# Optimization experiments

Measured on AMD Instinct MI355X. Metric: run time of the kernel, lower is better.

The kernel has to match this reference:

```python
import jax, jax.numpy as jnp
import numpy as np

N_NODES = 100000
FEAT_DIM = 256
MAX_DEG = 128
BATCH = 512          # per side (batch1, batch2)
S1 = 10              # layer-2 fanout (1-hop samples)
S2 = 25              # layer-1 fanout (2-hop samples)
HID = 256            # per-branch output dim; concat -> 512


def setup_inputs() -> dict:
    key = jax.random.key(0)
    ks = jax.random.split(key, 10)
    return {
        "features": jax.random.normal(ks[0], (N_NODES, FEAT_DIM), jnp.float32),
        "Ws1": jax.random.normal(ks[1], (FEAT_DIM, HID), jnp.float32) * 0.05,
        "Wn1": jax.random.normal(ks[2], (FEAT_DIM, HID), jnp.float32) * 0.05,
        "Ws2": jax.random.normal(ks[3], (2 * HID, HID), jnp.float32) * 0.05,
        "Wn2": jax.random.normal(ks[4], (2 * HID, HID), jnp.float32) * 0.05,
        "adj": jax.random.randint(ks[5], (N_NODES, MAX_DEG), 0, N_NODES, jnp.int32),
        "batch1": jax.random.randint(ks[6], (BATCH,), 0, N_NODES, jnp.int32),
        "batch2": jax.random.randint(ks[7], (BATCH,), 0, N_NODES, jnp.int32),
        "col1": jax.random.randint(ks[8], (2 * BATCH, S1), 0, MAX_DEG, jnp.int32),
        "col2": jax.random.randint(ks[9], (2 * BATCH * S1, S2), 0, MAX_DEG, jnp.int32),
    }


def _l2_normalize(x, eps=1e-12):
    return x * jax.lax.rsqrt(jnp.maximum(jnp.sum(x * x, axis=1, keepdims=True), eps))


def _mean_agg(h_self, h_neigh, fanout, Ws, Wn, act):
    # h_self: [M, d_in]; h_neigh: [M*fanout, d_in]
    neigh_mean = h_neigh.reshape(h_self.shape[0], fanout, -1).mean(axis=1)
    return act(jnp.concatenate([h_self @ Ws, neigh_mean @ Wn], axis=1))


def reference(features, Ws1, Wn1, Ws2, Wn2, adj, batch1, batch2, col1, col2):
    nodes = jnp.concatenate([batch1, batch2])                  # [2B]
    # uniform neighbor sampling via gather into preprocessed adjacency table
    s1 = jnp.take_along_axis(adj[nodes], col1, axis=1).reshape(-1)   # [2B*S1]
    s2 = jnp.take_along_axis(adj[s1], col2, axis=1).reshape(-1)      # [2B*S1*S2]
    h0 = features[nodes]      # [2B, D]
    h1 = features[s1]         # [2B*S1, D]
    h2 = features[s2]         # [2B*S1*S2, D]
    # GraphSAGE layer 1 (relu, concat)
    h0_new = _mean_agg(h0, h1, S1, Ws1, Wn1, jax.nn.relu)      # [2B, 2H]
    h1_new = _mean_agg(h1, h2, S2, Ws1, Wn1, jax.nn.relu)      # [2B*S1, 2H]
    # GraphSAGE layer 2 (identity act, concat)
    out = _mean_agg(h0_new, h1_new, S1, Ws2, Wn2, lambda x: x)  # [2B, 2H]
    out = _l2_normalize(out)
    return out  # rows [:BATCH] = outputs1, rows [BATCH:] = outputs2
```

## Files before the change

kernel.cpp:

```cpp
#include <hip/hip_runtime.h>
#include <hip/hip_bf16.h>

#define NB2    1024
#define FS1    10
#define FS2    25
#define FD     256
#define FH     256
#define MAXDEG 128

typedef __attribute__((ext_vector_type(8))) short bf16x8;
typedef __attribute__((ext_vector_type(4))) float f32x4;

__device__ inline ushort f2bf(float f) {
    union { float f; unsigned u; } v; v.f = f;
    unsigned u = v.u;
    unsigned r = (u + 0x7FFFu + ((u >> 16) & 1u)) >> 16;
    return (ushort)r;
}
__device__ inline float bf2f(ushort h) {
    union { unsigned u; float f; } v; v.u = ((unsigned)h) << 16;
    return v.f;
}

__global__ void prep_kernel(const float* __restrict__ Ws1, const float* __restrict__ Wn1,
                            const float* __restrict__ Ws2, const float* __restrict__ Wn2,
                            ushort* __restrict__ Wt_s1, ushort* __restrict__ Wt_n1,
                            ushort* __restrict__ Wt_s2, ushort* __restrict__ Wt_n2,
                            const int* __restrict__ batch1, const int* __restrict__ batch2,
                            const int* __restrict__ adj,
                            const int* __restrict__ col1, const int* __restrict__ col2,
                            int* __restrict__ nodes, int* __restrict__ s1,
                            int* __restrict__ s2)
{
    int b = blockIdx.x;
    if (b < 1536) {
        int t = b * 256 + threadIdx.x;
        const float* W; ushort* Wt; int K; int base;
        if (t < 131072) {
            K = 256;
            if (t < 65536) { W = Ws1; Wt = Wt_s1; base = 0; }
            else           { W = Wn1; Wt = Wt_n1; base = 65536; }
        } else {
            K = 512;
            if (t < 262144) { W = Ws2; Wt = Wt_s2; base = 131072; }
            else            { W = Wn2; Wt = Wt_n2; base = 262144; }
        }
        int tt = t - base;
        int k = tt >> 8;
        int n = tt & 255;
        Wt[(long)n * K + k] = f2bf(W[tt]);
    } else {
        int t2 = (b - 1536) * 256 + threadIdx.x;
        int i  = t2 / FS2;
        int ns = i / FS1;
        int node = (ns < 512) ? batch1[ns] : batch2[ns - 512];
        int s1v = adj[(long)node * MAXDEG + col1[i]];
        s2[t2] = adj[(long)s1v * MAXDEG + col2[t2]];
        if (t2 - i * FS2 == 0) {
            s1[i] = s1v;
            if (i - ns * FS1 == 0) nodes[ns] = node;
        }
    }
}

template<int F>
__device__ __forceinline__ void mean_body(const float* __restrict__ src,
                                          const int* __restrict__ idx,
                                          ushort* __restrict__ dst,
                                          int g, int l)
{
    const int* ip = idx + (long)g * F;
    int r[F];
    #pragma unroll
    for (int j = 0; j < F; ++j) r[j] = ip[j];

    float4 acc[4];
    #pragma unroll
    for (int q = 0; q < 4; ++q) acc[q] = make_float4(0.f, 0.f, 0.f, 0.f);

    #pragma unroll
    for (int j0 = 0; j0 < F; j0 += 8) {
        float4 v[8];
        #pragma unroll
        for (int u = 0; u < 8; ++u)
            if (j0 + u < F)
                v[u] = *((const float4*)(src + (long)r[j0 + u] * FD) + l);
        #pragma unroll
        for (int u = 0; u < 8; ++u)
            if (j0 + u < F) {
                int q = u & 3;
                acc[q].x += v[u].x; acc[q].y += v[u].y;
                acc[q].z += v[u].z; acc[q].w += v[u].w;
            }
    }
    float s = 1.0f / F;
    float sx = (acc[0].x + acc[1].x + acc[2].x + acc[3].x) * s;
    float sy = (acc[0].y + acc[1].y + acc[2].y + acc[3].y) * s;
    float sz = (acc[0].z + acc[1].z + acc[2].z + acc[3].z) * s;
    float sw = (acc[0].w + acc[1].w + acc[2].w + acc[3].w) * s;
    uint2 o;
    o.x = (unsigned)f2bf(sx) | ((unsigned)f2bf(sy) << 16);
    o.y = (unsigned)f2bf(sz) | ((unsigned)f2bf(sw) << 16);
    *((uint2*)(dst + (long)g * FD) + l) = o;
}

__device__ __forceinline__ void l1gemm_self_wave(const float* __restrict__ features,
                                                 const int* __restrict__ idx,
                                                 const ushort* __restrict__ Bt,
                                                 ushort* __restrict__ C,
                                                 int r0, int cs, int coff,
                                                 int m16, int g)
{
    const int row = r0 + m16;
    const long arow = (long)idx[row];

    f32x4 acc[4];
    #pragma unroll
    for (int j = 0; j < 4; ++j) acc[j] = (f32x4){0.f, 0.f, 0.f, 0.f};

    #pragma unroll
    for (int k0 = 0; k0 < 256; k0 += 32) {
        const float* p = features + arow * FD + k0 + g * 8;
        float4 v0 = *(const float4*)p;
        float4 v1 = *(const float4*)(p + 4);
        bf16x8 a;
        a[0] = (short)f2bf(v0.x); a[1] = (short)f2bf(v0.y);
        a[2] = (short)f2bf(v0.z); a[3] = (short)f2bf(v0.w);
        a[4] = (short)f2bf(v1.x); a[5] = (short)f2bf(v1.y);
        a[6] = (short)f2bf(v1.z); a[7] = (short)f2bf(v1.w);
        #pragma unroll
        for (int j = 0; j < 4; ++j) {
            bf16x8 bf = *(const bf16x8*)(Bt + (long)(cs * 64 + j * 16 + m16) * 256 + k0 + g * 8);
            acc[j] = __builtin_amdgcn_mfma_f32_16x16x32_bf16(a, bf, acc[j], 0, 0, 0);
        }
    }
    #pragma unroll
    for (int j = 0; j < 4; ++j)
        #pragma unroll
        for (int r = 0; r < 4; ++r)
            C[(long)(r0 + g * 4 + r) * 512 + coff + cs * 64 + j * 16 + m16] =
                f2bf(fmaxf(acc[j][r], 0.f));
}

__device__ __forceinline__ void l1gemm_neigh_wave(const ushort* __restrict__ An,
                                                  const ushort* __restrict__ Bt,
                                                  ushort* __restrict__ C,
                                                  int r0, int cs, int coff,
                                                  int m16, int g)
{
    const int row = r0 + m16;
    f32x4 acc[4];
    #pragma unroll
    for (int j = 0; j < 4; ++j) acc[j] = (f32x4){0.f, 0.f, 0.f, 0.f};

    #pragma unroll
    for (int k0 = 0; k0 < 256; k0 += 32) {
        bf16x8 a = *(const bf16x8*)(An + (long)row * FD + k0 + g * 8);
        #pragma unroll
        for (int j = 0; j < 4; ++j) {
            bf16x8 bf = *(const bf16x8*)(Bt + (long)(cs * 64 + j * 16 + m16) * 256 + k0 + g * 8);
            acc[j] = __builtin_amdgcn_mfma_f32_16x16x32_bf16(a, bf, acc[j], 0, 0, 0);
        }
    }
    #pragma unroll
    for (int j = 0; j < 4; ++j)
        #pragma unroll
        for (int r = 0; r < 4; ++r)
            C[(long)(r0 + g * 4 + r) * 512 + coff + cs * 64 + j * 16 + m16] =
                f2bf(fmaxf(acc[j][r], 0.f));
}

__device__ __forceinline__ void l2gemm_wave(const ushort* __restrict__ A,
                                            const ushort* __restrict__ Bt,
                                            float* __restrict__ op,
                                            int r0, int cs, int kh, int coff,
                                            int m16, int g)
{
    const int row = r0 + m16;
    const int kb  = kh * 128;
    f32x4 acc[4];
    #pragma unroll
    for (int j = 0; j < 4; ++j) acc[j] = (f32x4){0.f, 0.f, 0.f, 0.f};

    #pragma unroll
    for (int ks = 0; ks < 128; ks += 32) {
        int k = kb + ks;
        bf16x8 a = *(const bf16x8*)(A + (long)row * 512 + k + g * 8);
        #pragma unroll
        for (int j = 0; j < 4; ++j) {
            bf16x8 bf = *(const bf16x8*)(Bt + (long)(cs * 64 + j * 16 + m16) * 512 + k + g * 8);
            acc[j] = __builtin_amdgcn_mfma_f32_16x16x32_bf16(a, bf, acc[j], 0, 0, 0);
        }
    }
    #pragma unroll
    for (int j = 0; j < 4; ++j)
        #pragma unroll
        for (int r = 0; r < 4; ++r)
            op[(long)(r0 + g * 4 + r) * 512 + coff + cs * 64 + j * 16 + m16] = acc[j][r];
}

__global__ void k2_means_l1self(const float* __restrict__ features,
                                const int* __restrict__ s2, const int* __restrict__ s1,
                                const int* __restrict__ nodes,
                                ushort* __restrict__ nm2, ushort* __restrict__ nm1,
                                const ushort* __restrict__ Wt_s1,
                                ushort* __restrict__ h1n, ushort* __restrict__ h0n)
{
    int b = blockIdx.x;
    int wave = threadIdx.x >> 6;
    int l = threadIdx.x & 63;
    if (b < 2560) { mean_body<FS2>(features, s2, nm2, b * 4 + wave, l); return; }
    if (b < 2816) { mean_body<FS1>(features, s1, nm1, (b - 2816 + 256) * 4 + wave, l); return; }
    int u = (b - 2816) * 4 + wave;
    int cs = u & 3;
    int t = u >> 2;
    int m16 = l & 15, g = l >> 4;
    if (t < 640) l1gemm_self_wave(features, s1,    Wt_s1, h1n, t * 16,        cs, 0, m16, g);
    else         l1gemm_self_wave(features, nodes, Wt_s1, h0n, (t - 640) * 16, cs, 0, m16, g);
}

__global__ void k3_l1neigh(const ushort* __restrict__ nm2, const ushort* __restrict__ nm1,
                           const ushort* __restrict__ Wt_n1,
                           ushort* __restrict__ h1n, ushort* __restrict__ h0n)
{
    int u = blockIdx.x * 4 + (threadIdx.x >> 6);
    int l = threadIdx.x & 63;
    int cs = u & 3;
    int t = u >> 2;
    int m16 = l & 15, g = l >> 4;
    if (t < 640) l1gemm_neigh_wave(nm2, Wt_n1, h1n, t * 16,        cs, 256, m16, g);
    else         l1gemm_neigh_wave(nm1, Wt_n1, h0n, (t - 640) * 16, cs, 256, m16, g);
}

__global__ void k4_ml2_l2self(const ushort* __restrict__ h1n, ushort* __restrict__ ml2,
                              const ushort* __restrict__ h0n,
                              const ushort* __restrict__ Wt_s2,
                              float* __restrict__ opre)
{
    int b = blockIdx.x;
    int wave = threadIdx.x >> 6;
    int l = threadIdx.x & 63;
    if (b < 256) {
        int gp = b * 4 + wave;
        float acc[8] = {};
        for (int j = 0; j < FS1; ++j) {
            uint4 v = *((const uint4*)(h1n + ((long)gp * FS1 + j) * 512) + l);
            unsigned wd[4] = { v.x, v.y, v.z, v.w };
            #pragma unroll
            for (int q = 0; q < 4; ++q) {
                acc[2 * q]     += bf2f((ushort)(wd[q] & 0xFFFF));
                acc[2 * q + 1] += bf2f((ushort)(wd[q] >> 16));
            }
        }
        float s = 1.0f / FS1;
        uint4 o;
        unsigned* ow = (unsigned*)&o;
        #pragma unroll
        for (int q = 0; q < 4; ++q)
            ow[q] = (unsigned)f2bf(acc[2 * q] * s) | ((unsigned)f2bf(acc[2 * q + 1] * s) << 16);
        *((uint4*)(ml2 + (long)gp * 512) + l) = o;
        return;
    }
    int u = (b - 256) * 4 + wave;
    int kh = u & 3, cs = (u >> 2) & 3, rt = u >> 4;
    int m16 = l & 15, g = l >> 4;
    l2gemm_wave(h0n, Wt_s2, opre + (long)kh * NB2 * 512, rt * 16, cs, kh, 0, m16, g);
}

__global__ void k5_l2neigh(const ushort* __restrict__ ml2,
                           const ushort* __restrict__ Wt_n2,
                           float* __restrict__ opre)
{
    int u = blockIdx.x * 4 + (threadIdx.x >> 6);
    int l = threadIdx.x & 63;
    int kh = u & 3, cs = (u >> 2) & 3, rt = u >> 4;
    int m16 = l & 15, g = l >> 4;
    l2gemm_wave(ml2, Wt_n2, opre + (long)kh * NB2 * 512, rt * 16, cs, kh, 256, m16, g);
}

__global__ void l2norm_kernel(const float* __restrict__ in, float* __restrict__ out)
{
    int r = blockIdx.x;
    int t = threadIdx.x;
    long i0 = (long)r * 512 + t;
    const long P = (long)NB2 * 512;
    float v0 = in[i0]       + in[i0 + P]       + in[i0 + 2*P]       + in[i0 + 3*P];
    float v1 = in[i0 + 256] + in[i0 + P + 256] + in[i0 + 2*P + 256] + in[i0 + 3*P + 256];
    float s = v0 * v0 + v1 * v1;
    #pragma unroll
    for (int o = 32; o > 0; o >>= 1) s += __shfl_down(s, o, 64);
    __shared__ float wsum[4];
    if ((t & 63) == 0) wsum[t >> 6] = s;
    __syncthreads();
    float tot = wsum[0] + wsum[1] + wsum[2] + wsum[3];
    float inv = rsqrtf(fmaxf(tot, 1e-12f));
    out[r * 512 + t] = v0 * inv;
    out[r * 512 + 256 + t] = v1 * inv;
}

extern "C" void kernel_launch(void* const* d_in, const int* in_sizes, int n_in,
                              void* d_out, int out_size, void* d_ws, size_t ws_size,
                              hipStream_t stream)
{
    const float* features = (const float*)d_in[0];
    const float* Ws1      = (const float*)d_in[1];
    const float* Wn1      = (const float*)d_in[2];
    const float* Ws2      = (const float*)d_in[3];
    const float* Wn2      = (const float*)d_in[4];
    const int*   adj      = (const int*)d_in[5];
    const int*   batch1   = (const int*)d_in[6];
    const int*   batch2   = (const int*)d_in[7];
    const int*   col1     = (const int*)d_in[8];
    const int*   col2     = (const int*)d_in[9];
    float* out = (float*)d_out;

    char* w = (char*)d_ws;
    auto alloc = [&](size_t bytes) {
        char* p = w;
        w += (bytes + 255) & ~(size_t)255;
        return p;
    };
    int*    nodes = (int*)alloc((size_t)NB2 * 4);
    int*    s1    = (int*)alloc((size_t)NB2 * FS1 * 4);
    int*    s2    = (int*)alloc((size_t)NB2 * FS1 * FS2 * 4);
    ushort* nm1   = (ushort*)alloc((size_t)NB2 * FD * 2);
    ushort* nm2   = (ushort*)alloc((size_t)NB2 * FS1 * FD * 2);
    ushort* h0n   = (ushort*)alloc((size_t)NB2 * 512 * 2);
    ushort* h1n   = (ushort*)alloc((size_t)NB2 * FS1 * 512 * 2);
    ushort* ml2   = (ushort*)alloc((size_t)NB2 * 512 * 2);
    float*  opre  = (float*)alloc((size_t)4 * NB2 * 512 * 4);
    ushort* Wt_s1 = (ushort*)alloc((size_t)FD * FH * 2);
    ushort* Wt_n1 = (ushort*)alloc((size_t)FD * FH * 2);
    ushort* Wt_s2 = (ushort*)alloc((size_t)512 * FH * 2);
    ushort* Wt_n2 = (ushort*)alloc((size_t)512 * FH * 2);

    prep_kernel<<<2536, 256, 0, stream>>>(Ws1, Wn1, Ws2, Wn2,
                                          Wt_s1, Wt_n1, Wt_s2, Wt_n2,
                                          batch1, batch2, adj, col1, col2,
                                          nodes, s1, s2);

    k2_means_l1self<<<3520, 256, 0, stream>>>(features, s2, s1, nodes,
                                              nm2, nm1, Wt_s1, h1n, h0n);

    k3_l1neigh<<<704, 256, 0, stream>>>(nm2, nm1, Wt_n1, h1n, h0n);

    k4_ml2_l2self<<<512, 256, 0, stream>>>(h1n, ml2, h0n, Wt_s2, opre);

    k5_l2neigh<<<256, 256, 0, stream>>>(ml2, Wt_n2, opre);

    l2norm_kernel<<<NB2, 256, 0, stream>>>(opre, out);
}
```

Baseline: 98.68 us.

## Pre-convert feature table to bf16 and fuse layer-2 neighbor mean into GEMM

The prep kernel now converts the whole 100000x256 fp32 feature table to bf16 on every call. The mean and self-GEMM gathers then read half as many bytes and skip the per-element conversion. Separately, the layer-2 neighbor mean is computed inside the neighbor GEMM, with both layer-2 GEMMs in one kernel, which removes the ml2 buffer and one launch. The trade-off is a full-table read and write in the prep kernel, which is far more traffic than the gathers it saves. Neighbor means are also now summed from bf16-rounded inputs rather than fp32.

```diff
diff --git a/kernel.cpp b/kernel.cpp
--- a/kernel.cpp
+++ b/kernel.cpp
@@ -22,7 +22,8 @@
     return v.f;
 }
 
-__global__ void prep_kernel(const float* __restrict__ Ws1, const float* __restrict__ Wn1,
+__global__ void prep_kernel(const float* __restrict__ features, ushort* __restrict__ fbf,
+                            const float* __restrict__ Ws1, const float* __restrict__ Wn1,
                             const float* __restrict__ Ws2, const float* __restrict__ Wn2,
                             ushort* __restrict__ Wt_s1, ushort* __restrict__ Wt_n1,
                             ushort* __restrict__ Wt_s2, ushort* __restrict__ Wt_n2,
@@ -33,8 +34,15 @@
                             int* __restrict__ s2)
 {
     int b = blockIdx.x;
-    if (b < 1536) {
-        int t = b * 256 + threadIdx.x;
+    if (b < 25000) {
+        long t = (long)b * 256 + threadIdx.x;
+        float4 v = ((const float4*)features)[t];
+        uint2 o;
+        o.x = (unsigned)f2bf(v.x) | ((unsigned)f2bf(v.y) << 16);
+        o.y = (unsigned)f2bf(v.z) | ((unsigned)f2bf(v.w) << 16);
+        ((uint2*)fbf)[t] = o;
+    } else if (b < 26536) {
+        int t = (b - 25000) * 256 + threadIdx.x;
         const float* W; ushort* Wt; int K; int base;
         if (t < 131072) {
             K = 256;
@@ -50,7 +58,7 @@
         int n = tt & 255;
         Wt[(long)n * K + k] = f2bf(W[tt]);
     } else {
-        int t2 = (b - 1536) * 256 + threadIdx.x;
+        int t2 = (b - 26536) * 256 + threadIdx.x;
         int i  = t2 / FS2;
         int ns = i / FS1;
         int node = (ns < 512) ? batch1[ns] : batch2[ns - 512];
@@ -64,7 +72,7 @@
 }
 
 template<int F>
-__device__ __forceinline__ void mean_body(const float* __restrict__ src,
+__device__ __forceinline__ void mean_body(const ushort* __restrict__ src,
                                           const int* __restrict__ idx,
                                           ushort* __restrict__ dst,
                                           int g, int l)
@@ -74,37 +82,32 @@
     #pragma unroll
     for (int j = 0; j < F; ++j) r[j] = ip[j];
 
-    float4 acc[4];
-    #pragma unroll
-    for (int q = 0; q < 4; ++q) acc[q] = make_float4(0.f, 0.f, 0.f, 0.f);
+    float acc[4] = {0.f, 0.f, 0.f, 0.f};
 
     #pragma unroll
     for (int j0 = 0; j0 < F; j0 += 8) {
-        float4 v[8];
+        uint2 v[8];
         #pragma unroll
         for (int u = 0; u < 8; ++u)
             if (j0 + u < F)
-                v[u] = *((const float4*)(src + (long)r[j0 + u] * FD) + l);
+                v[u] = *((const uint2*)(src + (long)r[j0 + u] * FD) + l);
         #pragma unroll
         for (int u = 0; u < 8; ++u)
             if (j0 + u < F) {
-                int q = u & 3;
-                acc[q].x += v[u].x; acc[q].y += v[u].y;
-                acc[q].z += v[u].z; acc[q].w += v[u].w;
+                acc[0] += bf2f((ushort)(v[u].x & 0xFFFF));
+                acc[1] += bf2f((ushort)(v[u].x >> 16));
+                acc[2] += bf2f((ushort)(v[u].y & 0xFFFF));
+                acc[3] += bf2f((ushort)(v[u].y >> 16));
             }
     }
     float s = 1.0f / F;
-    float sx = (acc[0].x + acc[1].x + acc[2].x + acc[3].x) * s;
-    float sy = (acc[0].y + acc[1].y + acc[2].y + acc[3].y) * s;
-    float sz = (acc[0].z + acc[1].z + acc[2].z + acc[3].z) * s;
-    float sw = (acc[0].w + acc[1].w + acc[2].w + acc[3].w) * s;
     uint2 o;
-    o.x = (unsigned)f2bf(sx) | ((unsigned)f2bf(sy) << 16);
-    o.y = (unsigned)f2bf(sz) | ((unsigned)f2bf(sw) << 16);
+    o.x = (unsigned)f2bf(acc[0] * s) | ((unsigned)f2bf(acc[1] * s) << 16);
+    o.y = (unsigned)f2bf(acc[2] * s) | ((unsigned)f2bf(acc[3] * s) << 16);
     *((uint2*)(dst + (long)g * FD) + l) = o;
 }
 
-__device__ __forceinline__ void l1gemm_self_wave(const float* __restrict__ features,
+__device__ __forceinline__ void l1gemm_self_wave(const ushort* __restrict__ fbf,
                                                  const int* __restrict__ idx,
                                                  const ushort* __restrict__ Bt,
                                                  ushort* __restrict__ C,
@@ -120,14 +123,7 @@
 
     #pragma unroll
     for (int k0 = 0; k0 < 256; k0 += 32) {
-        const float* p = features + arow * FD + k0 + g * 8;
-        float4 v0 = *(const float4*)p;
-        float4 v1 = *(const float4*)(p + 4);
-        bf16x8 a;
-        a[0] = (short)f2bf(v0.x); a[1] = (short)f2bf(v0.y);
-        a[2] = (short)f2bf(v0.z); a[3] = (short)f2bf(v0.w);
-        a[4] = (short)f2bf(v1.x); a[5] = (short)f2bf(v1.y);
-        a[6] = (short)f2bf(v1.z); a[7] = (short)f2bf(v1.w);
+        bf16x8 a = *(const bf16x8*)(fbf + arow * FD + k0 + g * 8);
         #pragma unroll
         for (int j = 0; j < 4; ++j) {
             bf16x8 bf = *(const bf16x8*)(Bt + (long)(cs * 64 + j * 16 + m16) * 256 + k0 + g * 8);
@@ -199,7 +195,7 @@
             op[(long)(r0 + g * 4 + r) * 512 + coff + cs * 64 + j * 16 + m16] = acc[j][r];
 }
 
-__global__ void k2_means_l1self(const float* __restrict__ features,
+__global__ void k2_means_l1self(const ushort* __restrict__ fbf,
                                 const int* __restrict__ s2, const int* __restrict__ s1,
                                 const int* __restrict__ nodes,
                                 ushort* __restrict__ nm2, ushort* __restrict__ nm1,
@@ -209,14 +205,14 @@
     int b = blockIdx.x;
     int wave = threadIdx.x >> 6;
     int l = threadIdx.x & 63;
-    if (b < 2560) { mean_body<FS2>(features, s2, nm2, b * 4 + wave, l); return; }
-    if (b < 2816) { mean_body<FS1>(features, s1, nm1, (b - 2816 + 256) * 4 + wave, l); return; }
+    if (b < 2560) { mean_body<FS2>(fbf, s2, nm2, b * 4 + wave, l); return; }
+    if (b < 2816) { mean_body<FS1>(fbf, s1, nm1, (b - 2560) * 4 + wave, l); return; }
     int u = (b - 2816) * 4 + wave;
     int cs = u & 3;
     int t = u >> 2;
     int m16 = l & 15, g = l >> 4;
-    if (t < 640) l1gemm_self_wave(features, s1,    Wt_s1, h1n, t * 16,        cs, 0, m16, g);
-    else         l1gemm_self_wave(features, nodes, Wt_s1, h0n, (t - 640) * 16, cs, 0, m16, g);
+    if (t < 640) l1gemm_self_wave(fbf, s1,    Wt_s1, h1n, t * 16,         cs, 0, m16, g);
+    else         l1gemm_self_wave(fbf, nodes, Wt_s1, h0n, (t - 640) * 16, cs, 0, m16, g);
 }
 
 __global__ void k3_l1neigh(const ushort* __restrict__ nm2, const ushort* __restrict__ nm1,
@@ -228,54 +224,63 @@
     int cs = u & 3;
     int t = u >> 2;
     int m16 = l & 15, g = l >> 4;
-    if (t < 640) l1gemm_neigh_wave(nm2, Wt_n1, h1n, t * 16,        cs, 256, m16, g);
+    if (t < 640) l1gemm_neigh_wave(nm2, Wt_n1, h1n, t * 16,         cs, 256, m16, g);
     else         l1gemm_neigh_wave(nm1, Wt_n1, h0n, (t - 640) * 16, cs, 256, m16, g);
 }
 
-__global__ void k4_ml2_l2self(const ushort* __restrict__ h1n, ushort* __restrict__ ml2,
-                              const ushort* __restrict__ h0n,
-                              const ushort* __restrict__ Wt_s2,
-                              float* __restrict__ opre)
+__global__ void k4_l2both(const ushort* __restrict__ h1n, const ushort* __restrict__ h0n,
+                          const ushort* __restrict__ Wt_s2, const ushort* __restrict__ Wt_n2,
+                          float* __restrict__ opre)
 {
     int b = blockIdx.x;
     int wave = threadIdx.x >> 6;
     int l = threadIdx.x & 63;
+    int m16 = l & 15, g = l >> 4;
     if (b < 256) {
-        int gp = b * 4 + wave;
-        float acc[8] = {};
+        int u = b * 4 + wave;
+        int kh = u & 3, cs = (u >> 2) & 3, rt = u >> 4;
+        l2gemm_wave(h0n, Wt_s2, opre + (long)kh * NB2 * 512, rt * 16, cs, kh, 0, m16, g);
+        return;
+    }
+    int u = (b - 256) * 4 + wave;
+    int kh = u & 3, cs = (u >> 2) & 3, rt = u >> 4;
+    const int r0  = rt * 16;
+    const int row = r0 + m16;
+    const int kb  = kh * 128;
+
+    f32x4 acc[4];
+    #pragma unroll
+    for (int j = 0; j < 4; ++j) acc[j] = (f32x4){0.f, 0.f, 0.f, 0.f};
+
+    #pragma unroll
+    for (int ks = 0; ks < 128; ks += 32) {
+        int k = kb + ks;
+        float a8[8] = {};
+        #pragma unroll
         for (int j = 0; j < FS1; ++j) {
-            uint4 v = *((const uint4*)(h1n + ((long)gp * FS1 + j) * 512) + l);
+            uint4 v = *(const uint4*)(h1n + ((long)row * FS1 + j) * 512 + k + g * 8);
             unsigned wd[4] = { v.x, v.y, v.z, v.w };
             #pragma unroll
             for (int q = 0; q < 4; ++q) {
-                acc[2 * q]     += bf2f((ushort)(wd[q] & 0xFFFF));
-                acc[2 * q + 1] += bf2f((ushort)(wd[q] >> 16));
+                a8[2 * q]     += bf2f((ushort)(wd[q] & 0xFFFF));
+                a8[2 * q + 1] += bf2f((ushort)(wd[q] >> 16));
             }
         }
-        float s = 1.0f / FS1;
-        uint4 o;
-        unsigned* ow = (unsigned*)&o;
-        #pragma unroll
-        for (int q = 0; q < 4; ++q)
-            ow[q] = (unsigned)f2bf(acc[2 * q] * s) | ((unsigned)f2bf(acc[2 * q + 1] * s) << 16);
-        *((uint4*)(ml2 + (long)gp * 512) + l) = o;
-        return;
-    }
-    int u = (b - 256) * 4 + wave;
-    int kh = u & 3, cs = (u >> 2) & 3, rt = u >> 4;
-    int m16 = l & 15, g = l >> 4;
-    l2gemm_wave(h0n, Wt_s2, opre + (long)kh * NB2 * 512, rt * 16, cs, kh, 0, m16, g);
-}
-
-__global__ void k5_l2neigh(const ushort* __restrict__ ml2,
-                           const ushort* __restrict__ Wt_n2,
-                           float* __restrict__ opre)
-{
-    int u = blockIdx.x * 4 + (threadIdx.x >> 6);
-    int l = threadIdx.x & 63;
-    int kh = u & 3, cs = (u >> 2) & 3, rt = u >> 4;
-    int m16 = l & 15, g = l >> 4;
-    l2gemm_wave(ml2, Wt_n2, opre + (long)kh * NB2 * 512, rt * 16, cs, kh, 256, m16, g);
+        bf16x8 a;
+        #pragma unroll
+        for (int q = 0; q < 8; ++q) a[q] = (short)f2bf(a8[q] * (1.0f / FS1));
+        #pragma unroll
+        for (int j = 0; j < 4; ++j) {
+            bf16x8 bf = *(const bf16x8*)(Wt_n2 + (long)(cs * 64 + j * 16 + m16) * 512 + k + g * 8);
+            acc[j] = __builtin_amdgcn_mfma_f32_16x16x32_bf16(a, bf, acc[j], 0, 0, 0);
+        }
+    }
+    float* op = opre + (long)kh * NB2 * 512;
+    #pragma unroll
+    for (int j = 0; j < 4; ++j)
+        #pragma unroll
+        for (int r = 0; r < 4; ++r)
+            op[(long)(r0 + g * 4 + r) * 512 + 256 + cs * 64 + j * 16 + m16] = acc[j][r];
 }
 
 __global__ void l2norm_kernel(const float* __restrict__ in, float* __restrict__ out)
@@ -320,6 +325,7 @@
         w += (bytes + 255) & ~(size_t)255;
         return p;
     };
+    ushort* fbf   = (ushort*)alloc((size_t)100000 * FD * 2);
     int*    nodes = (int*)alloc((size_t)NB2 * 4);
     int*    s1    = (int*)alloc((size_t)NB2 * FS1 * 4);
     int*    s2    = (int*)alloc((size_t)NB2 * FS1 * FS2 * 4);
@@ -327,26 +333,23 @@
     ushort* nm2   = (ushort*)alloc((size_t)NB2 * FS1 * FD * 2);
     ushort* h0n   = (ushort*)alloc((size_t)NB2 * 512 * 2);
     ushort* h1n   = (ushort*)alloc((size_t)NB2 * FS1 * 512 * 2);
-    ushort* ml2   = (ushort*)alloc((size_t)NB2 * 512 * 2);
     float*  opre  = (float*)alloc((size_t)4 * NB2 * 512 * 4);
     ushort* Wt_s1 = (ushort*)alloc((size_t)FD * FH * 2);
     ushort* Wt_n1 = (ushort*)alloc((size_t)FD * FH * 2);
     ushort* Wt_s2 = (ushort*)alloc((size_t)512 * FH * 2);
     ushort* Wt_n2 = (ushort*)alloc((size_t)512 * FH * 2);
 
-    prep_kernel<<<2536, 256, 0, stream>>>(Ws1, Wn1, Ws2, Wn2,
-                                          Wt_s1, Wt_n1, Wt_s2, Wt_n2,
-                                          batch1, batch2, adj, col1, col2,
-                                          nodes, s1, s2);
-
-    k2_means_l1self<<<3520, 256, 0, stream>>>(features, s2, s1, nodes,
+    prep_kernel<<<27536, 256, 0, stream>>>(features, fbf, Ws1, Wn1, Ws2, Wn2,
+                                           Wt_s1, Wt_n1, Wt_s2, Wt_n2,
+                                           batch1, batch2, adj, col1, col2,
+                                           nodes, s1, s2);
+
+    k2_means_l1self<<<3520, 256, 0, stream>>>(fbf, s2, s1, nodes,
                                               nm2, nm1, Wt_s1, h1n, h0n);
 
     k3_l1neigh<<<704, 256, 0, stream>>>(nm2, nm1, Wt_n1, h1n, h0n);
 
-    k4_ml2_l2self<<<512, 256, 0, stream>>>(h1n, ml2, h0n, Wt_s2, opre);
-
-    k5_l2neigh<<<256, 256, 0, stream>>>(ml2, Wt_n2, opre);
+    k4_l2both<<<512, 256, 0, stream>>>(h1n, h0n, Wt_s2, Wt_n2, opre);
 
     l2norm_kernel<<<NB2, 256, 0, stream>>>(opre, out);
 }
```

New measurement: 103.3 us. 1.05x slower.
